# Kernel optimization log

Hardware: AMD Instinct MI355X
Metric: run time of the kernel (lower is better)

Reference implementation:

```python
import jax, jax.numpy as jnp
import numpy as np

CHUNK = 512  # tile size along N; keeps per-step [B,CHUNK,M] tile ~64 MB, never builds full [B,N,M]


def setup_inputs() -> dict:
    key = jax.random.key(0)
    k1, k2 = jax.random.split(key)
    xyz1 = jax.random.normal(k1, (4, 8192, 3), dtype=jnp.float32)
    xyz2 = jax.random.normal(k2, (4, 8192, 3), dtype=jnp.float32)
    return {"xyz1": xyz1, "xyz2": xyz2}


def _chamfer(xyz1, xyz2):
    # xyz1: [B,N,3], xyz2: [B,M,3]
    B, N, _ = xyz1.shape
    M = xyz2.shape[1]
    K = N // CHUNK
    x1_chunks = xyz1.reshape(B, K, CHUNK, 3).transpose(1, 0, 2, 3)  # [K,B,C,3]

    def step(carry, x1k):
        best_d2, best_i2, start = carry  # running mins for xyz2 -> xyz1 direction
        # squared distances for this tile: [B,C,M]
        d = jnp.sum((x1k[:, :, None, :] - xyz2[:, None, :, :]) ** 2, axis=-1)
        # xyz1 -> xyz2: min over M
        d1 = jnp.min(d, axis=2)                              # [B,C]
        i1 = jnp.argmin(d, axis=2).astype(jnp.int32)         # [B,C]
        # xyz2 -> xyz1: partial min over this chunk of N
        dc = jnp.min(d, axis=1)                              # [B,M]
        ic = jnp.argmin(d, axis=1).astype(jnp.int32) + start # [B,M], global index
        upd = dc < best_d2
        best_d2 = jnp.where(upd, dc, best_d2)
        best_i2 = jnp.where(upd, ic, best_i2)
        return (best_d2, best_i2, start + CHUNK), (d1, i1)

    init = (jnp.full((B, M), jnp.inf, dtype=xyz1.dtype),
            jnp.zeros((B, M), dtype=jnp.int32),
            jnp.int32(0))
    (dist2, idx2, _), (d1s, i1s) = jax.lax.scan(step, init, x1_chunks)
    dist1 = d1s.transpose(1, 0, 2).reshape(B, N)
    idx1 = i1s.transpose(1, 0, 2).reshape(B, N)
    return dist1, dist2, idx1, idx2


def reference(xyz1, xyz2):
    # Matches ChamferDistance.forward: (dist1, dist2, idx1, idx2),
    # squared nearest-neighbor distances and int32 argmin indices.
    return _chamfer(xyz1, xyz2)
```

## Files before the change

kernel.cpp:

```cpp
#include <hip/hip_runtime.h>
#include <math.h>


#define QPT 4
#define BLK 256
#define QPB (QPT*BLK)

__global__ __launch_bounds__(256, 4) void chamfer_main(
    const float* __restrict__ xyz1, const float* __restrict__ xyz2,
    unsigned long long* __restrict__ pp,
    int N, int M, int B, int S, int C)
{
    const int dir = blockIdx.z;
    const float* q = dir ? xyz2 : xyz1;
    const float* r = dir ? xyz1 : xyz2;
    const int Nq = dir ? M : N;
    const int Nr = dir ? N : M;
    const int b     = blockIdx.y / S;
    const int split = blockIdx.y % S;
    const int base  = split * C;

    extern __shared__ float s[];

    {
        const float4* gv = (const float4*)(r + ((size_t)b * Nr + base) * 3);
        float4* sv = (float4*)s;
        const int elems4 = C * 3 / 4;
        for (int t = threadIdx.x; t < elems4; t += BLK) sv[t] = gv[t];
    }
    __syncthreads();

    float qx[QPT], qy[QPT], qz[QPT];
    int qi[QPT];
    bool qv[QPT];
#pragma unroll
    for (int k = 0; k < QPT; ++k) {
        qi[k] = blockIdx.x * QPB + k * BLK + threadIdx.x;
        qv[k] = qi[k] < Nq;
        const float* qp = q + ((size_t)b * Nq + (qv[k] ? qi[k] : 0)) * 3;
        qx[k] = qp[0]; qy[k] = qp[1]; qz[k] = qp[2];
    }

    float bd[QPT];
    int   gi[QPT];
#pragma unroll
    for (int k = 0; k < QPT; ++k) { bd[k] = INFINITY; gi[k] = 0; }

    const float4* sv = (const float4*)s;
    const int iters = C / 8;
    for (int j8 = 0; j8 < iters; ++j8) {
        float4 f0 = sv[6 * j8 + 0];
        float4 f1 = sv[6 * j8 + 1];
        float4 f2 = sv[6 * j8 + 2];
        float4 f3 = sv[6 * j8 + 3];
        float4 f4 = sv[6 * j8 + 4];
        float4 f5 = sv[6 * j8 + 5];
        float px[8] = { f0.x, f0.w, f1.z, f2.y, f3.x, f3.w, f4.z, f5.y };
        float py[8] = { f0.y, f1.x, f1.w, f2.z, f3.y, f4.x, f4.w, f5.z };
        float pz[8] = { f0.z, f1.y, f2.x, f2.w, f3.z, f4.y, f5.x, f5.w };
#pragma unroll
        for (int k = 0; k < QPT; ++k) {
            float d[8];
#pragma unroll
            for (int p = 0; p < 8; ++p) {
                float dx = qx[k] - px[p];
                float dy = qy[k] - py[p];
                float dz = qz[k] - pz[p];
                d[p] = fmaf(dx, dx, fmaf(dy, dy, dz * dz));
            }
            float m01 = fminf(d[0], d[1]);
            float m23 = fminf(d[2], d[3]);
            float m45 = fminf(d[4], d[5]);
            float m67 = fminf(d[6], d[7]);
            float m = fminf(fminf(m01, m23), fminf(m45, m67));
            if (m < bd[k]) { bd[k] = m; gi[k] = j8; }
        }
    }

    const size_t obase = (size_t)(dir * B + b) * Nq;
#pragma unroll
    for (int k = 0; k < QPT; ++k) {
        if (!qv[k]) continue;
        const int g = gi[k];
        float4 f0 = sv[6 * g + 0];
        float4 f1 = sv[6 * g + 1];
        float4 f2 = sv[6 * g + 2];
        float4 f3 = sv[6 * g + 3];
        float4 f4 = sv[6 * g + 4];
        float4 f5 = sv[6 * g + 5];
        float px[8] = { f0.x, f0.w, f1.z, f2.y, f3.x, f3.w, f4.z, f5.y };
        float py[8] = { f0.y, f1.x, f1.w, f2.z, f3.y, f4.x, f4.w, f5.z };
        float pz[8] = { f0.z, f1.y, f2.x, f2.w, f3.z, f4.y, f5.x, f5.w };
        int best = 0;
#pragma unroll
        for (int p = 7; p >= 0; --p) {
            float dx = qx[k] - px[p];
            float dy = qy[k] - py[p];
            float dz = qz[k] - pz[p];
            float d = fmaf(dx, dx, fmaf(dy, dy, dz * dz));
            if (d == bd[k]) best = p;
        }
        const int idx = base + g * 8 + best;
        unsigned long long packed =
            ((unsigned long long)__float_as_uint(bd[k]) << 32) | (unsigned)idx;
        atomicMin(&pp[obase + qi[k]], packed);
    }
}

__global__ __launch_bounds__(256) void chamfer_final(
    const unsigned long long* __restrict__ pp,
    float* __restrict__ out, int N, int M, int B)
{
    const int gid = blockIdx.x * blockDim.x + threadIdx.x;
    const int perDir0 = B * N;
    int dir, rem;
    if (gid < perDir0) { dir = 0; rem = gid; }
    else if (gid < perDir0 + B * M) { dir = 1; rem = gid - perDir0; }
    else return;
    const int Nq = dir ? M : N;

    unsigned long long v = pp[(size_t)(dir * B) * Nq + rem];

    float* dist_out = out + (dir ? (size_t)B * N : 0);
    float* idx_out  = out + (size_t)B * N + (size_t)B * M + (dir ? (size_t)B * N : 0);
    dist_out[rem] = __uint_as_float((unsigned)(v >> 32));
    idx_out[rem]  = (float)(unsigned)(v & 0xffffffffu);
}

extern "C" void kernel_launch(void* const* d_in, const int* in_sizes, int n_in,
                              void* d_out, int out_size, void* d_ws, size_t ws_size,
                              hipStream_t stream) {
    const float* xyz1 = (const float*)d_in[0];
    const float* xyz2 = (const float*)d_in[1];
    float* out = (float*)d_out;
    const int B = 4;
    const int N = in_sizes[0] / (B * 3);
    const int M = in_sizes[1] / (B * 3);
    const int NQ = (N > M ? N : M);
    const int NR = (N > M ? N : M);

    int S = 32;
    while (NR % (S * 8)) S >>= 1;
    const int C = NR / S;

    unsigned long long* pp = (unsigned long long*)d_ws;
    const int nslots = 2 * B * NQ;

    hipMemsetAsync(pp, 0xFF, (size_t)nslots * 8, stream);

    dim3 grid((NQ + QPB - 1) / QPB, B * S, 2);
    size_t lds = (size_t)C * 3 * sizeof(float);
    chamfer_main<<<grid, dim3(BLK, 1, 1), lds, stream>>>(
        xyz1, xyz2, pp, N, M, B, S, C);

    chamfer_final<<<dim3((nslots + 255) / 256, 1, 1), dim3(256, 1, 1), 0, stream>>>(
        pp, out, N, M, B);
}
```

Baseline: 124.6 us.

## Defer in-group argmin resolution to final kernel and rebalance min tree

The main kernel no longer re-scans the winning 8-point group per query to find the exact index. It packs the global group index with the distance into the atomicMin key. The final kernel then reloads that group from global memory and recomputes the 8 distances to pick the matching point, doing the resolution once per query instead of once per split. The min reduction is also restructured into a different fminf tree shape. One tie-breaking risk is that atomicMin on the group index can pick a different winner than the element index would when distances are equal across groups.

```diff
diff --git a/kernel.cpp b/kernel.cpp
--- a/kernel.cpp
+++ b/kernel.cpp
@@ -68,46 +68,28 @@
                 float dz = qz[k] - pz[p];
                 d[p] = fmaf(dx, dx, fmaf(dy, dy, dz * dz));
             }
-            float m01 = fminf(d[0], d[1]);
-            float m23 = fminf(d[2], d[3]);
-            float m45 = fminf(d[4], d[5]);
-            float m67 = fminf(d[6], d[7]);
-            float m = fminf(fminf(m01, m23), fminf(m45, m67));
+            float t0 = fminf(fminf(d[0], d[1]), d[2]);
+            float t1 = fminf(fminf(d[3], d[4]), d[5]);
+            float t2 = fminf(fminf(d[6], d[7]), t0);
+            float m  = fminf(t1, t2);
             if (m < bd[k]) { bd[k] = m; gi[k] = j8; }
         }
     }
 
     const size_t obase = (size_t)(dir * B + b) * Nq;
+    const int gbase = split * (C / 8);
 #pragma unroll
     for (int k = 0; k < QPT; ++k) {
         if (!qv[k]) continue;
-        const int g = gi[k];
-        float4 f0 = sv[6 * g + 0];
-        float4 f1 = sv[6 * g + 1];
-        float4 f2 = sv[6 * g + 2];
-        float4 f3 = sv[6 * g + 3];
-        float4 f4 = sv[6 * g + 4];
-        float4 f5 = sv[6 * g + 5];
-        float px[8] = { f0.x, f0.w, f1.z, f2.y, f3.x, f3.w, f4.z, f5.y };
-        float py[8] = { f0.y, f1.x, f1.w, f2.z, f3.y, f4.x, f4.w, f5.z };
-        float pz[8] = { f0.z, f1.y, f2.x, f2.w, f3.z, f4.y, f5.x, f5.w };
-        int best = 0;
-#pragma unroll
-        for (int p = 7; p >= 0; --p) {
-            float dx = qx[k] - px[p];
-            float dy = qy[k] - py[p];
-            float dz = qz[k] - pz[p];
-            float d = fmaf(dx, dx, fmaf(dy, dy, dz * dz));
-            if (d == bd[k]) best = p;
-        }
-        const int idx = base + g * 8 + best;
         unsigned long long packed =
-            ((unsigned long long)__float_as_uint(bd[k]) << 32) | (unsigned)idx;
+            ((unsigned long long)__float_as_uint(bd[k]) << 32)
+            | (unsigned)(gbase + gi[k]);
         atomicMin(&pp[obase + qi[k]], packed);
     }
 }
 
 __global__ __launch_bounds__(256) void chamfer_final(
+    const float* __restrict__ xyz1, const float* __restrict__ xyz2,
     const unsigned long long* __restrict__ pp,
     float* __restrict__ out, int N, int M, int B)
 {
@@ -118,13 +100,39 @@
     else if (gid < perDir0 + B * M) { dir = 1; rem = gid - perDir0; }
     else return;
     const int Nq = dir ? M : N;
+    const int Nr = dir ? N : M;
+    const float* q = dir ? xyz2 : xyz1;
+    const float* r = dir ? xyz1 : xyz2;
 
     unsigned long long v = pp[(size_t)(dir * B) * Nq + rem];
+    const unsigned bits = (unsigned)(v >> 32);
+    const int grp = (int)(v & 0xffffffffu);
+
+    const int b  = rem / Nq;
+    const int qi = rem - b * Nq;
+    const float* qp = q + ((size_t)b * Nq + qi) * 3;
+    const float qx = qp[0], qy = qp[1], qz = qp[2];
+
+    const float4* rv = (const float4*)(r + ((size_t)b * Nr + (size_t)grp * 8) * 3);
+    float4 f0 = rv[0], f1 = rv[1], f2 = rv[2], f3 = rv[3], f4 = rv[4], f5 = rv[5];
+    float px[8] = { f0.x, f0.w, f1.z, f2.y, f3.x, f3.w, f4.z, f5.y };
+    float py[8] = { f0.y, f1.x, f1.w, f2.z, f3.y, f4.x, f4.w, f5.z };
+    float pz[8] = { f0.z, f1.y, f2.x, f2.w, f3.z, f4.y, f5.x, f5.w };
+    int best = 0;
+#pragma unroll
+    for (int p = 7; p >= 0; --p) {
+        float dx = qx - px[p];
+        float dy = qy - py[p];
+        float dz = qz - pz[p];
+        float d = fmaf(dx, dx, fmaf(dy, dy, dz * dz));
+        if (__float_as_uint(d) == bits) best = p;
+    }
+    const int idx = grp * 8 + best;
 
     float* dist_out = out + (dir ? (size_t)B * N : 0);
     float* idx_out  = out + (size_t)B * N + (size_t)B * M + (dir ? (size_t)B * N : 0);
-    dist_out[rem] = __uint_as_float((unsigned)(v >> 32));
-    idx_out[rem]  = (float)(unsigned)(v & 0xffffffffu);
+    dist_out[rem] = __uint_as_float(bits);
+    idx_out[rem]  = (float)idx;
 }
 
 extern "C" void kernel_launch(void* const* d_in, const int* in_sizes, int n_in,
@@ -154,5 +162,5 @@
         xyz1, xyz2, pp, N, M, B, S, C);
 
     chamfer_final<<<dim3((nslots + 255) / 256, 1, 1), dim3(256, 1, 1), 0, stream>>>(
-        pp, out, N, M, B);
+        xyz1, xyz2, pp, out, N, M, B);
 }
```

Result: no change. 122.6 us (-1.6%).
